# Kernel tuning notes

Hardware: AMD Instinct MI355X
Metric: run time of the kernel (lower is better)

The kernel has to match this reference:

```python
import jax, jax.numpy as jnp
import numpy as np

EPSILON = 0.1      # entropic regularization
N_ITERS = 50       # Sinkhorn fixed-point iterations
EPS_STAB = 1e-6    # numerical stabilizer (max(eps_stab, 1e-6) in original)
N, M, D = 8192, 8192, 128


def _sinkhorn_cost(X, Y):
    # squared Euclidean cost matrix (n, m)
    x2 = jnp.sum(X * X, axis=-1)
    y2 = jnp.sum(Y * Y, axis=-1)
    C = jnp.maximum(x2[:, None] + y2[None, :] - 2.0 * (X @ Y.T), 0.0)
    K = jnp.exp(-C / EPSILON)
    n, m = X.shape[0], Y.shape[0]
    a = jnp.full((n,), 1.0 / n, dtype=C.dtype)
    b = jnp.full((m,), 1.0 / m, dtype=C.dtype)

    def step(uv, _):
        u, v = uv
        Kv = K @ v + EPS_STAB
        u = jnp.where(jnp.abs(Kv) < EPS_STAB, a, a / jnp.maximum(Kv, EPS_STAB))
        Ktu = K.T @ u + EPS_STAB
        v = jnp.where(jnp.abs(Ktu) < EPS_STAB, b, b / jnp.maximum(Ktu, EPS_STAB))
        return (u, v), None

    (u, v), _ = jax.lax.scan(step, (jnp.ones_like(a), jnp.ones_like(b)), None, length=N_ITERS)
    # cost = sum(pi * C) with pi = u[:,None] * K * v[None,:], fused via einsum
    return jnp.einsum('i,ij,ij,j->', u, K, C, v)


def setup_inputs() -> dict:
    key = jax.random.key(0)
    k1, k2 = jax.random.split(key)
    # scale so squared distances ~O(1), commensurate with EPSILON
    X = jax.random.normal(k1, (N, D), dtype=jnp.float32) * 0.05
    Y = jax.random.normal(k2, (M, D), dtype=jnp.float32) * 0.05
    return {"X": X, "Y": Y}


def reference(X, Y):
    ot_xy = _sinkhorn_cost(X, Y)
    ot_xx = _sinkhorn_cost(X, jax.lax.stop_gradient(X))
    ot_yy = _sinkhorn_cost(Y, jax.lax.stop_gradient(Y))
    div = ot_xy - 0.5 * (ot_xx + ot_yy)
    div = jnp.where(jnp.isfinite(div), div, jnp.zeros_like(div))
    return jnp.maximum(div, 0.0)
```

## Files before the change

### kernel.cpp

```cpp
#include <hip/hip_runtime.h>

#define NPTS 8192
#define DIM  128
#define WPREP(x) (0.015625f / ((x) + 1.28e-4f))

typedef short s16x8 __attribute__((ext_vector_type(8)));
typedef float f32x4 __attribute__((ext_vector_type(4)));
typedef float f32x2 __attribute__((ext_vector_type(2)));

__device__ __forceinline__ ushort f2bf(float f) {
  unsigned u = __float_as_uint(f);
  u += 0x7fffu + ((u >> 16) & 1u);
  return (ushort)(u >> 16);
}
__device__ __forceinline__ float bf2f(ushort b) {
  return __uint_as_float(((unsigned)b) << 16);
}

__device__ __forceinline__ unsigned char fp8_enc_sw(float f) {
  if (f < 0.015625f) {
    int mi = (int)rintf(f * 512.0f);
    return (unsigned char)(mi >= 8 ? 0x08 : mi);
  }
  unsigned u = __float_as_uint(f);
  unsigned r = u + 0xfffffu + ((u >> 20) & 1u);
  int e = (int)((r >> 23) & 0xff) - 127;
  unsigned mant = (r >> 20) & 7u;
  if (e > 8 || (e == 8 && mant > 6)) return 0x7e;
  return (unsigned char)(((e + 7) << 3) | mant);
}
__device__ __forceinline__ float fp8_dec_sw(unsigned b) {
  unsigned E = (b >> 3) & 15u, M = b & 7u;
  float n = __uint_as_float(((E + 120u) << 23) | (M << 20));
  float s = (float)M * 0.001953125f;
  return E ? n : s;
}
__device__ __forceinline__ unsigned char enc1(float f) {
#if __has_builtin(__builtin_amdgcn_cvt_pk_fp8_f32)
  return (unsigned char)(__builtin_amdgcn_cvt_pk_fp8_f32(f, f, 0, false) & 0xff);
#else
  return fp8_enc_sw(f);
#endif
}
template <bool HI>
__device__ __forceinline__ f32x2 dec2(unsigned w) {
#if __has_builtin(__builtin_amdgcn_cvt_pk_f32_fp8)
  return __builtin_amdgcn_cvt_pk_f32_fp8((int)w, HI);
#else
  f32x2 r;
  r.x = fp8_dec_sw(HI ? ((w >> 16) & 0xffu) : (w & 0xffu));
  r.y = fp8_dec_sw(HI ? (w >> 24) : ((w >> 8) & 0xffu));
  return r;
#endif
}

__device__ __forceinline__ int swz(int j) { return j + 2 * (j >> 5); }
#define WSZ (NPTS + 2 * (NPTS / 32) + 8)

__global__ __launch_bounds__(256) void init_zero2(float* __restrict__ a,
                                                  float* __restrict__ b) {
  int j = blockIdx.x * 256 + threadIdx.x;
  a[j] = 0.0f; b[j] = 0.0f;
}

__global__ __launch_bounds__(256) void sq_rows(const float* __restrict__ X,
                                               const float* __restrict__ Y,
                                               float* __restrict__ x2,
                                               float* __restrict__ y2) {
  int wave = threadIdx.x >> 6, lane = threadIdx.x & 63;
  int row = blockIdx.x * 4 + wave;
  const float* src = (row < NPTS) ? X + (size_t)row * DIM
                                  : Y + (size_t)(row - NPTS) * DIM;
  float2 v = *reinterpret_cast<const float2*>(src + lane * 2);
  float ax = bf2f(f2bf(v.x)), ay = bf2f(f2bf(v.y));
  float s = ax * ax + ay * ay;
  for (int off = 32; off; off >>= 1) s += __shfl_down(s, off, 64);
  if (lane == 0) {
    if (row < NPTS) x2[row] = s; else y2[row - NPTS] = s;
  }
}

__global__ __launch_bounds__(256) void build_k(const float* __restrict__ A,
                                               const float* __restrict__ B,
                                               const float* __restrict__ a2,
                                               const float* __restrict__ b2,
                                               unsigned char* __restrict__ K8) {
  __shared__ ushort At[128][136];
  __shared__ ushort Bt[128][136];
  int t = threadIdx.x;
  int tm = blockIdx.x, tn = blockIdx.y;
  {
    int r = t >> 1;
    int c0 = (t & 1) * 64;
    const float* Ar = A + (size_t)(tm * 128 + r) * DIM + c0;
    const float* Br = B + (size_t)(tn * 128 + r) * DIM + c0;
    for (int c = 0; c < 64; c += 4) {
      float4 av = *reinterpret_cast<const float4*>(Ar + c);
      float4 bv = *reinterpret_cast<const float4*>(Br + c);
      unsigned pa0 = (unsigned)f2bf(av.x) | ((unsigned)f2bf(av.y) << 16);
      unsigned pa1 = (unsigned)f2bf(av.z) | ((unsigned)f2bf(av.w) << 16);
      unsigned pb0 = (unsigned)f2bf(bv.x) | ((unsigned)f2bf(bv.y) << 16);
      unsigned pb1 = (unsigned)f2bf(bv.z) | ((unsigned)f2bf(bv.w) << 16);
      *reinterpret_cast<unsigned*>(&At[r][c0 + c + 0]) = pa0;
      *reinterpret_cast<unsigned*>(&At[r][c0 + c + 2]) = pa1;
      *reinterpret_cast<unsigned*>(&Bt[r][c0 + c + 0]) = pb0;
      *reinterpret_cast<unsigned*>(&Bt[r][c0 + c + 2]) = pb1;
    }
  }
  __syncthreads();
  int wave = t >> 6, lane = t & 63;
  int lr = lane & 15;
  int lk = (lane >> 4) * 8;
  f32x4 acc[2][8];
  for (int mi = 0; mi < 2; ++mi)
    for (int ni = 0; ni < 8; ++ni)
      acc[mi][ni] = (f32x4){0.f, 0.f, 0.f, 0.f};
  for (int kc = 0; kc < 4; ++kc) {
    s16x8 af[2], bfr[8];
    af[0] = *reinterpret_cast<const s16x8*>(&At[wave * 32 + lr][kc * 32 + lk]);
    af[1] = *reinterpret_cast<const s16x8*>(&At[wave * 32 + 16 + lr][kc * 32 + lk]);
    for (int ni = 0; ni < 8; ++ni)
      bfr[ni] = *reinterpret_cast<const s16x8*>(&Bt[ni * 16 + lr][kc * 32 + lk]);
    for (int mi = 0; mi < 2; ++mi)
      for (int ni = 0; ni < 8; ++ni)
        acc[mi][ni] = __builtin_amdgcn_mfma_f32_16x16x32_bf16(af[mi], bfr[ni],
                                                              acc[mi][ni], 0, 0, 0);
  }
  int drow = (lane >> 4) * 4;
  float a2r[2][4], b2c[8];
  for (int mi = 0; mi < 2; ++mi)
    for (int r = 0; r < 4; ++r) a2r[mi][r] = a2[tm * 128 + wave * 32 + mi * 16 + drow + r];
  for (int ni = 0; ni < 8; ++ni) b2c[ni] = b2[tn * 128 + ni * 16 + lr];
  __syncthreads();
  unsigned char (*O)[144] = reinterpret_cast<unsigned char (*)[144]>(&At[0][0]);
  for (int mi = 0; mi < 2; ++mi)
    for (int ni = 0; ni < 8; ++ni)
      for (int r = 0; r < 4; ++r) {
        float S = acc[mi][ni][r];
        float C = fmaxf(a2r[mi][r] + b2c[ni] - 2.0f * S, 0.0f);
        float kv = exp2f(7.0f - 14.426950408889634f * C);
        O[wave * 32 + mi * 16 + drow + r][ni * 16 + lr] = enc1(kv);
      }
  __syncthreads();
  int row = t >> 1, half = t & 1;
  const uint4* src = reinterpret_cast<const uint4*>(&O[row][half * 64]);
  uint4* dst = reinterpret_cast<uint4*>(K8 + (size_t)(tm * 128 + row) * NPTS + tn * 128 + half * 64);
#pragma unroll
  for (int k = 0; k < 4; ++k) dst[k] = src[k];
}

struct SymMem {
  unsigned char T[128][132];
  float wj[128], wi[128];
  float cp[8][128];
};

__device__ __forceinline__ void sym_tile(const unsigned char* __restrict__ K8,
                                         const float* __restrict__ in,
                                         float* __restrict__ acc,
                                         float* __restrict__ zn,
                                         int tid, int init, SymMem& sm) {
  int t = threadIdx.x;
  if (tid < 32) zn[tid * 256 + t] = 0.0f;
  int bi = (int)(64.5f - sqrtf(64.5f * 64.5f - 2.0f * (float)tid));
  if (bi < 0) bi = 0; if (bi > 63) bi = 63;
  while (bi > 0 && tid < bi * 64 - bi * (bi - 1) / 2) --bi;
  while (tid >= (bi + 1) * 64 - (bi + 1) * bi / 2) ++bi;
  int bj = bi + tid - (bi * 64 - bi * (bi - 1) / 2);
  if (t < 128) sm.wj[t] = init ? 1.0f : WPREP(in[bj * 128 + t]);
  else         sm.wi[t - 128] = init ? 1.0f : WPREP(in[bi * 128 + (t - 128)]);
  int r = t >> 1, h = t & 1;
  const unsigned char* src = K8 + (size_t)(bi * 128 + r) * NPTS + bj * 128 + h * 64;
  uint4 q[4];
#pragma unroll
  for (int k = 0; k < 4; ++k) q[k] = *reinterpret_cast<const uint4*>(src + 16 * k);
  bool offdiag = (bi != bj);
  if (offdiag) {
#pragma unroll
    for (int k = 0; k < 4; ++k)
      *reinterpret_cast<uint4*>(&sm.T[r][h * 64 + 16 * k]) = q[k];
  }
  __syncthreads();
  float racc = 0.f;
#pragma unroll
  for (int k = 0; k < 4; ++k) {
    const unsigned* p = &q[k].x;
#pragma unroll
    for (int e = 0; e < 4; ++e) {
      f32x2 lo = dec2<false>(p[e]), hi2 = dec2<true>(p[e]);
      int c = h * 64 + k * 16 + e * 4;
      racc = fmaf(lo.x, sm.wj[c], racc);
      racc = fmaf(lo.y, sm.wj[c + 1], racc);
      racc = fmaf(hi2.x, sm.wj[c + 2], racc);
      racc = fmaf(hi2.y, sm.wj[c + 3], racc);
    }
  }
  racc += __shfl_xor(racc, 1, 64);
  if (h == 0) atomicAdd(&acc[bi * 128 + r], racc);
  if (offdiag) {
    int cg = t >> 3, rg = t & 7;
    float c0 = 0.f, c1 = 0.f, c2 = 0.f, c3 = 0.f;
#pragma unroll
    for (int i = 0; i < 16; ++i) {
      int row = rg * 16 + ((i + rg * 2) & 15);
      unsigned v = *reinterpret_cast<const unsigned*>(&sm.T[row][cg * 4]);
      float wr = sm.wi[row];
      f32x2 lo = dec2<false>(v), hi2 = dec2<true>(v);
      c0 = fmaf(lo.x, wr, c0);
      c1 = fmaf(lo.y, wr, c1);
      c2 = fmaf(hi2.x, wr, c2);
      c3 = fmaf(hi2.y, wr, c3);
    }
    *reinterpret_cast<float4*>(&sm.cp[rg][cg * 4]) = make_float4(c0, c1, c2, c3);
    __syncthreads();
    if (t < 128) {
      float s = (((sm.cp[0][t] + sm.cp[1][t]) + (sm.cp[2][t] + sm.cp[3][t])) +
                 ((sm.cp[4][t] + sm.cp[5][t]) + (sm.cp[6][t] + sm.cp[7][t])));
      atomicAdd(&acc[bj * 128 + t], s);
    }
  }
}

__device__ __forceinline__ void row_block(const unsigned char* __restrict__ K8,
                                          float* __restrict__ out,
                                          int row0, int t, const float* w) {
  int lane = t & 63;
  const unsigned char* K0 = K8 + (size_t)row0 * NPTS + lane * 16;
  const unsigned char* K1 = K0 + NPTS;
  float a0 = 0.f, b0 = 0.f, a1 = 0.f, b1 = 0.f;
  uint4 c0 = *reinterpret_cast<const uint4*>(K0);
  uint4 c1 = *reinterpret_cast<const uint4*>(K1);
#pragma unroll
  for (int rnd = 0; rnd < 8; ++rnd) {
    uint4 n0 = c0, n1 = c1;
    if (rnd < 7) {
      n0 = *reinterpret_cast<const uint4*>(K0 + (rnd + 1) * 1024);
      n1 = *reinterpret_cast<const uint4*>(K1 + (rnd + 1) * 1024);
    }
    int pb = swz(rnd * 1024 + lane * 16);
    const unsigned* p0 = &c0.x;
    const unsigned* p1 = &c1.x;
#pragma unroll
    for (int e = 0; e < 4; ++e) {
      f32x2 w0 = *reinterpret_cast<const f32x2*>(&w[pb + 4 * e]);
      f32x2 w1 = *reinterpret_cast<const f32x2*>(&w[pb + 4 * e + 2]);
      f32x2 k0l = dec2<false>(p0[e]), k0h = dec2<true>(p0[e]);
      f32x2 k1l = dec2<false>(p1[e]), k1h = dec2<true>(p1[e]);
      a0 = fmaf(k0l.x, w0.x, a0); b0 = fmaf(k0l.y, w0.y, b0);
      a0 = fmaf(k0h.x, w1.x, a0); b0 = fmaf(k0h.y, w1.y, b0);
      a1 = fmaf(k1l.x, w0.x, a1); b1 = fmaf(k1l.y, w0.y, b1);
      a1 = fmaf(k1h.x, w1.x, a1); b1 = fmaf(k1h.y, w1.y, b1);
    }
    c0 = n0; c1 = n1;
  }
  float s0 = a0 + b0, s1 = a1 + b1;
  for (int off = 32; off; off >>= 1) {
    s0 += __shfl_down(s0, off, 64);
    s1 += __shfl_down(s1, off, 64);
  }
  if (lane == 0) { out[row0] = s0; out[row0 + 1] = s1; }
}

union MegaMem {
  SymMem sym;
  float w[WSZ];
  float us[64];
};

__global__ __launch_bounds__(256) void megapass(const unsigned char* __restrict__ KA,
                                                const unsigned char* __restrict__ KB,
                                                const unsigned char* __restrict__ KXY,
                                                const float* __restrict__ inA,
                                                const float* __restrict__ inB,
                                                float* __restrict__ accA,
                                                float* __restrict__ accB,
                                                float* __restrict__ znA,
                                                float* __restrict__ znB,
                                                const float* __restrict__ xyin,
                                                float* __restrict__ rxy,
                                                float* __restrict__ vabn,
                                                int p, int xyrole) {
  __shared__ MegaMem sm;
  int bx = blockIdx.x;
  int t = threadIdx.x;
  bool isxy = (bx % 5 == 4) && (bx < 5120);
  if (isxy) {
    int xyi = bx / 5;
    if (xyrole == 0) {
      if (t < 8) vabn[xyi * 8 + t] = 0.0f;
      if (p == 1) {
#pragma unroll
        for (int k = 0; k < 32; ++k) sm.w[swz(t + 256 * k)] = 1.0f;
      } else {
        float tmp[32];
#pragma unroll
        for (int k = 0; k < 32; ++k) tmp[k] = xyin[t + 256 * k];
#pragma unroll
        for (int k = 0; k < 32; ++k) sm.w[swz(t + 256 * k)] = WPREP(tmp[k]);
      }
      __syncthreads();
      int row0 = xyi * 8 + (t >> 6) * 2;
      row_block(KXY, rxy, row0, t, sm.w);
    } else {
      int jb = xyi & 7, ic = xyi >> 3;
      int i0 = ic * 64;
      if (t < 64) sm.us[t] = WPREP(rxy[i0 + t]);
      __syncthreads();
      int j0 = jb * 1024 + t * 4;
      float acc0 = 0.f, acc1 = 0.f, acc2 = 0.f, acc3 = 0.f;
      for (int i = 0; i < 64; i += 8) {
        unsigned wv[8];
#pragma unroll
        for (int k = 0; k < 8; ++k)
          wv[k] = *reinterpret_cast<const unsigned*>(KXY + (size_t)(i0 + i + k) * NPTS + j0);
#pragma unroll
        for (int k = 0; k < 8; ++k) {
          float uu = sm.us[i + k];
          f32x2 lo = dec2<false>(wv[k]), hi = dec2<true>(wv[k]);
          acc0 = fmaf(lo.x, uu, acc0);
          acc1 = fmaf(lo.y, uu, acc1);
          acc2 = fmaf(hi.x, uu, acc2);
          acc3 = fmaf(hi.y, uu, acc3);
        }
      }
      atomicAdd(&vabn[j0 + 0], acc0);
      atomicAdd(&vabn[j0 + 1], acc1);
      atomicAdd(&vabn[j0 + 2], acc2);
      atomicAdd(&vabn[j0 + 3], acc3);
    }
  } else {
    int nxy_below = (bx < 5120) ? ((bx + 1) / 5) : 1024;
    int symi = bx - nxy_below;
    int half = symi & 1;
    int tid = symi >> 1;
    sym_tile(half ? KB : KA, half ? inB : inA, half ? accB : accA,
             half ? znB : znA, tid, p == 1 ? 1 : 0, sm.sym);
  }
}

__global__ __launch_bounds__(256) void sympass2(const unsigned char* __restrict__ KA,
                                                const unsigned char* __restrict__ KB,
                                                const float* __restrict__ inA,
                                                const float* __restrict__ inB,
                                                float* __restrict__ accA,
                                                float* __restrict__ accB,
                                                float* __restrict__ znA,
                                                float* __restrict__ znB,
                                                int init) {
  __shared__ SymMem sm;
  int half = blockIdx.y;
  sym_tile(half ? KB : KA, half ? inB : inA, half ? accB : accA,
           half ? znB : znA, blockIdx.x, init, sm);
}

__device__ __forceinline__ void prep_w512(float* w, const float* __restrict__ in, int init, int t) {
  if (init) {
#pragma unroll
    for (int k = 0; k < 16; ++k) w[swz(t + 512 * k)] = 1.0f;
  } else {
    float tmp[16];
#pragma unroll
    for (int k = 0; k < 16; ++k) tmp[k] = in[t + 512 * k];
#pragma unroll
    for (int k = 0; k < 16; ++k) w[swz(t + 512 * k)] = WPREP(tmp[k]);
  }
}

__global__ __launch_bounds__(512) void rowpass_xy(const unsigned char* __restrict__ K8,
                                                  const float* __restrict__ in,
                                                  float* __restrict__ out,
                                                  float* __restrict__ vzero,
                                                  int init) {
  __shared__ float w[WSZ];
  int t = threadIdx.x;
  if (t < 16) vzero[blockIdx.x * 16 + t] = 0.0f;
  prep_w512(w, in, init, t);
  __syncthreads();
  int row0 = blockIdx.x * 16 + (t >> 6) * 2;
  row_block(K8, out, row0, t, w);
}

__global__ __launch_bounds__(256) void colpass(const unsigned char* __restrict__ K8,
                                               const float* __restrict__ uraw,
                                               float* __restrict__ vout) {
  __shared__ float us[64];
  int t = threadIdx.x;
  int jb = blockIdx.x;
  int ic = blockIdx.y;
  int i0 = ic * 64;
  if (t < 64) us[t] = WPREP(uraw[i0 + t]);
  __syncthreads();
  int j0 = jb * 1024 + t * 4;
  float acc0 = 0.f, acc1 = 0.f, acc2 = 0.f, acc3 = 0.f;
  for (int i = 0; i < 64; i += 8) {
    unsigned wv[8];
#pragma unroll
    for (int k = 0; k < 8; ++k)
      wv[k] = *reinterpret_cast<const unsigned*>(K8 + (size_t)(i0 + i + k) * NPTS + j0);
#pragma unroll
    for (int k = 0; k < 8; ++k) {
      float uu = us[i + k];
      f32x2 lo = dec2<false>(wv[k]), hi = dec2<true>(wv[k]);
      acc0 = fmaf(lo.x, uu, acc0);
      acc1 = fmaf(lo.y, uu, acc1);
      acc2 = fmaf(hi.x, uu, acc2);
      acc3 = fmaf(hi.y, uu, acc3);
    }
  }
  atomicAdd(&vout[j0 + 0], acc0);
  atomicAdd(&vout[j0 + 1], acc1);
  atomicAdd(&vout[j0 + 2], acc2);
  atomicAdd(&vout[j0 + 3], acc3);
}

__global__ __launch_bounds__(256) void costpass(const unsigned char* __restrict__ K8,
                                                const float* __restrict__ uraw,
                                                const float* __restrict__ vraw,
                                                float* __restrict__ partial) {
  __shared__ float w[WSZ];
  __shared__ float wsum[4];
  int t = threadIdx.x;
  {
    float tmp[32];
#pragma unroll
    for (int k = 0; k < 32; ++k) tmp[k] = vraw[t + 256 * k];
#pragma unroll
    for (int k = 0; k < 32; ++k) w[swz(t + 256 * k)] = WPREP(tmp[k]);
  }
  __syncthreads();
  int wave = t >> 6, lane = t & 63;
  int row = blockIdx.x * 4 + wave;
  const unsigned char* Kr = K8 + (size_t)row * NPTS + lane * 16;
  float acc = 0.f;
  uint4 c = *reinterpret_cast<const uint4*>(Kr);
#pragma unroll
  for (int rnd = 0; rnd < 8; ++rnd) {
    uint4 n = c;
    if (rnd < 7) n = *reinterpret_cast<const uint4*>(Kr + (rnd + 1) * 1024);
    const unsigned* p = &c.x;
    int pb = swz(rnd * 1024 + lane * 16);
#pragma unroll
    for (int e = 0; e < 4; ++e) {
      f32x2 w0 = *reinterpret_cast<const f32x2*>(&w[pb + 4 * e]);
      f32x2 w1 = *reinterpret_cast<const f32x2*>(&w[pb + 4 * e + 2]);
      f32x2 kl = dec2<false>(p[e]), kh = dec2<true>(p[e]);
      float c0 = (kl.x > 0.f) ? 0.069314718f * (7.0f - __log2f(kl.x)) : 0.f;
      float c1 = (kl.y > 0.f) ? 0.069314718f * (7.0f - __log2f(kl.y)) : 0.f;
      float c2 = (kh.x > 0.f) ? 0.069314718f * (7.0f - __log2f(kh.x)) : 0.f;
      float c3 = (kh.y > 0.f) ? 0.069314718f * (7.0f - __log2f(kh.y)) : 0.f;
      acc = fmaf(kl.x * c0, w0.x, acc);
      acc = fmaf(kl.y * c1, w0.y, acc);
      acc = fmaf(kh.x * c2, w1.x, acc);
      acc = fmaf(kh.y * c3, w1.y, acc);
    }
    c = n;
  }
  for (int off = 32; off; off >>= 1) acc += __shfl_down(acc, off, 64);
  if (lane == 0) {
    float u = WPREP(uraw[row]);
    wsum[wave] = acc * u * 0.0078125f;
  }
  __syncthreads();
  if (t == 0) partial[blockIdx.x] = (wsum[0] + wsum[1]) + (wsum[2] + wsum[3]);
}

__global__ __launch_bounds__(256) void final_combine(const float* __restrict__ pxy,
                                                     const float* __restrict__ pxx,
                                                     const float* __restrict__ pyy,
                                                     float* __restrict__ out) {
  __shared__ float buf[3][256];
  int t = threadIdx.x;
  float s0 = 0.f, s1 = 0.f, s2 = 0.f;
  for (int i = t; i < 2048; i += 256) { s0 += pxy[i]; s1 += pxx[i]; s2 += pyy[i]; }
  buf[0][t] = s0; buf[1][t] = s1; buf[2][t] = s2;
  __syncthreads();
  for (int off = 128; off; off >>= 1) {
    if (t < off) {
      buf[0][t] += buf[0][t + off];
      buf[1][t] += buf[1][t + off];
      buf[2][t] += buf[2][t + off];
    }
    __syncthreads();
  }
  if (t == 0) {
    float div = buf[0][0] - 0.5f * (buf[1][0] + buf[2][0]);
    if (!isfinite(div)) div = 0.0f;
    out[0] = fmaxf(div, 0.0f);
  }
}

extern "C" void kernel_launch(void* const* d_in, const int* in_sizes, int n_in,
                              void* d_out, int out_size, void* d_ws, size_t ws_size,
                              hipStream_t stream) {
  const float* X = (const float*)d_in[0];
  const float* Y = (const float*)d_in[1];
  float* out = (float*)d_out;
  char* ws = (char*)d_ws;

  size_t off = 0;
  unsigned char* KA = (unsigned char*)(ws + off); off += (size_t)NPTS * NPTS;
  unsigned char* KB = (unsigned char*)(ws + off); off += (size_t)NPTS * NPTS;
  float* zA[3]; float* zB[3];
  for (int i = 0; i < 3; ++i) { zA[i] = (float*)(ws + off); off += (size_t)NPTS * 4; }
  for (int i = 0; i < 3; ++i) { zB[i] = (float*)(ws + off); off += (size_t)NPTS * 4; }
  float* rxy  = (float*)(ws + off); off += (size_t)NPTS * 4;
  float* vab0 = (float*)(ws + off); off += (size_t)NPTS * 4;
  float* vab1 = (float*)(ws + off); off += (size_t)NPTS * 4;
  float* x2   = (float*)(ws + off); off += (size_t)NPTS * 4;
  float* y2   = (float*)(ws + off); off += (size_t)NPTS * 4;
  float* pxy  = (float*)(ws + off); off += 2048 * 4;
  float* pxx  = (float*)(ws + off); off += 2048 * 4;
  float* pyy  = (float*)(ws + off); off += 2048 * 4;
  size_t need_base = off;
  unsigned char* KXY = (unsigned char*)(ws + off); off += (size_t)NPTS * NPTS;
  bool fused = (ws_size >= off);
  if (ws_size < need_base) {
    (void)hipMemsetAsync(d_out, 0, sizeof(float), stream);
    return;
  }
  float* vab[2] = {vab0, vab1};

  init_zero2<<<32, 256, 0, stream>>>(zA[1], zB[1]);
  sq_rows<<<4096, 256, 0, stream>>>(X, Y, x2, y2);

  if (fused) {
    build_k<<<dim3(64, 64), 256, 0, stream>>>(X, X, x2, x2, KA);
    build_k<<<dim3(64, 64), 256, 0, stream>>>(Y, Y, y2, y2, KB);
    build_k<<<dim3(64, 64), 256, 0, stream>>>(X, Y, x2, y2, KXY);
    for (int k = 0; k < 100; ++k) {
      int p = k + 1;
      int it = k >> 1;
      int role = k & 1;
      megapass<<<5184, 256, 0, stream>>>(KA, KB, KXY,
                                         zA[(p - 1) % 3], zB[(p - 1) % 3],
                                         zA[p % 3], zB[p % 3],
                                         zA[(p + 1) % 3], zB[(p + 1) % 3],
                                         vab[it & 1], rxy, vab[(it + 1) & 1],
                                         p, role);
    }
    costpass<<<2048, 256, 0, stream>>>(KA, zA[0], zA[1], pxx);
    costpass<<<2048, 256, 0, stream>>>(KB, zB[0], zB[1], pyy);
    costpass<<<2048, 256, 0, stream>>>(KXY, rxy, vab[0], pxy);
  } else {
    build_k<<<dim3(64, 64), 256, 0, stream>>>(X, X, x2, x2, KA);
    build_k<<<dim3(64, 64), 256, 0, stream>>>(Y, Y, y2, y2, KB);
    for (int p = 1; p <= 100; ++p) {
      sympass2<<<dim3(2080, 2), 256, 0, stream>>>(KA, KB,
                                                  zA[(p - 1) % 3], zB[(p - 1) % 3],
                                                  zA[p % 3], zB[p % 3],
                                                  zA[(p + 1) % 3], zB[(p + 1) % 3],
                                                  p == 1 ? 1 : 0);
    }
    costpass<<<2048, 256, 0, stream>>>(KA, zA[0], zA[1], pxx);
    costpass<<<2048, 256, 0, stream>>>(KB, zB[0], zB[1], pyy);
    build_k<<<dim3(64, 64), 256, 0, stream>>>(X, Y, x2, y2, KA);
    for (int it = 0; it < 50; ++it) {
      rowpass_xy<<<512, 512, 0, stream>>>(KA, vab[it & 1], rxy,
                                          vab[(it + 1) & 1], it == 0 ? 1 : 0);
      colpass<<<dim3(8, 128), 256, 0, stream>>>(KA, rxy, vab[(it + 1) & 1]);
    }
    costpass<<<2048, 256, 0, stream>>>(KA, rxy, vab[0], pxy);
  }

  final_combine<<<1, 256, 0, stream>>>(pxy, pxx, pyy, out);
}
```

Baseline: 3.312 ms.

## Chunk XY weight staging in LDS, add occupancy hint, and XOR-swizzle build_k tiles

The XY row-block path of megapass no longer stages the full 8192-entry weight vector in shared memory. It now streams it in double-buffered 2048-entry chunks, interleaving the weight loads with the FP8 K row dot products. This shrinks LDS use, and together with a launch_bounds minimum-blocks hint of 6 it aims to raise occupancy for the memory-bound sweeps, at the cost of extra barriers. Separately, build_k XOR-swizzles the bf16 tile columns in LDS to reduce bank conflicts on the MFMA fragment loads.

```diff
diff --git a/kernel.cpp b/kernel.cpp
--- a/kernel.cpp
+++ b/kernel.cpp
@@ -56,6 +56,7 @@
 
 __device__ __forceinline__ int swz(int j) { return j + 2 * (j >> 5); }
 #define WSZ (NPTS + 2 * (NPTS / 32) + 8)
+#define CHSZ 2176
 
 __global__ __launch_bounds__(256) void init_zero2(float* __restrict__ a,
                                                   float* __restrict__ b) {
@@ -92,6 +93,7 @@
   {
     int r = t >> 1;
     int c0 = (t & 1) * 64;
+    int xr = (r & 7) << 4;
     const float* Ar = A + (size_t)(tm * 128 + r) * DIM + c0;
     const float* Br = B + (size_t)(tn * 128 + r) * DIM + c0;
     for (int c = 0; c < 64; c += 4) {
@@ -101,26 +103,29 @@
       unsigned pa1 = (unsigned)f2bf(av.z) | ((unsigned)f2bf(av.w) << 16);
       unsigned pb0 = (unsigned)f2bf(bv.x) | ((unsigned)f2bf(bv.y) << 16);
       unsigned pb1 = (unsigned)f2bf(bv.z) | ((unsigned)f2bf(bv.w) << 16);
-      *reinterpret_cast<unsigned*>(&At[r][c0 + c + 0]) = pa0;
-      *reinterpret_cast<unsigned*>(&At[r][c0 + c + 2]) = pa1;
-      *reinterpret_cast<unsigned*>(&Bt[r][c0 + c + 0]) = pb0;
-      *reinterpret_cast<unsigned*>(&Bt[r][c0 + c + 2]) = pb1;
+      int cc = (c0 + c) ^ xr;
+      *reinterpret_cast<unsigned*>(&At[r][cc + 0]) = pa0;
+      *reinterpret_cast<unsigned*>(&At[r][cc + 2]) = pa1;
+      *reinterpret_cast<unsigned*>(&Bt[r][cc + 0]) = pb0;
+      *reinterpret_cast<unsigned*>(&Bt[r][cc + 2]) = pb1;
     }
   }
   __syncthreads();
   int wave = t >> 6, lane = t & 63;
   int lr = lane & 15;
   int lk = (lane >> 4) * 8;
+  int xs = (lr & 7) << 4;
   f32x4 acc[2][8];
   for (int mi = 0; mi < 2; ++mi)
     for (int ni = 0; ni < 8; ++ni)
       acc[mi][ni] = (f32x4){0.f, 0.f, 0.f, 0.f};
   for (int kc = 0; kc < 4; ++kc) {
+    int ck = (kc * 32 + lk) ^ xs;
     s16x8 af[2], bfr[8];
-    af[0] = *reinterpret_cast<const s16x8*>(&At[wave * 32 + lr][kc * 32 + lk]);
-    af[1] = *reinterpret_cast<const s16x8*>(&At[wave * 32 + 16 + lr][kc * 32 + lk]);
+    af[0] = *reinterpret_cast<const s16x8*>(&At[wave * 32 + lr][ck]);
+    af[1] = *reinterpret_cast<const s16x8*>(&At[wave * 32 + 16 + lr][ck]);
     for (int ni = 0; ni < 8; ++ni)
-      bfr[ni] = *reinterpret_cast<const s16x8*>(&Bt[ni * 16 + lr][kc * 32 + lk]);
+      bfr[ni] = *reinterpret_cast<const s16x8*>(&Bt[ni * 16 + lr][ck]);
     for (int mi = 0; mi < 2; ++mi)
       for (int ni = 0; ni < 8; ++ni)
         acc[mi][ni] = __builtin_amdgcn_mfma_f32_16x16x32_bf16(af[mi], bfr[ni],
@@ -263,23 +268,23 @@
 
 union MegaMem {
   SymMem sym;
-  float w[WSZ];
+  float wch[2][CHSZ];
   float us[64];
 };
 
-__global__ __launch_bounds__(256) void megapass(const unsigned char* __restrict__ KA,
-                                                const unsigned char* __restrict__ KB,
-                                                const unsigned char* __restrict__ KXY,
-                                                const float* __restrict__ inA,
-                                                const float* __restrict__ inB,
-                                                float* __restrict__ accA,
-                                                float* __restrict__ accB,
-                                                float* __restrict__ znA,
-                                                float* __restrict__ znB,
-                                                const float* __restrict__ xyin,
-                                                float* __restrict__ rxy,
-                                                float* __restrict__ vabn,
-                                                int p, int xyrole) {
+__global__ __launch_bounds__(256, 6) void megapass(const unsigned char* __restrict__ KA,
+                                                   const unsigned char* __restrict__ KB,
+                                                   const unsigned char* __restrict__ KXY,
+                                                   const float* __restrict__ inA,
+                                                   const float* __restrict__ inB,
+                                                   float* __restrict__ accA,
+                                                   float* __restrict__ accB,
+                                                   float* __restrict__ znA,
+                                                   float* __restrict__ znB,
+                                                   const float* __restrict__ xyin,
+                                                   float* __restrict__ rxy,
+                                                   float* __restrict__ vabn,
+                                                   int p, int xyrole) {
   __shared__ MegaMem sm;
   int bx = blockIdx.x;
   int t = threadIdx.x;
@@ -288,19 +293,73 @@
     int xyi = bx / 5;
     if (xyrole == 0) {
       if (t < 8) vabn[xyi * 8 + t] = 0.0f;
+      int lane = t & 63;
+      int row0 = xyi * 8 + (t >> 6) * 2;
+      const unsigned char* K0 = KXY + (size_t)row0 * NPTS + lane * 16;
+      const unsigned char* K1 = K0 + NPTS;
       if (p == 1) {
 #pragma unroll
-        for (int k = 0; k < 32; ++k) sm.w[swz(t + 256 * k)] = 1.0f;
+        for (int k = 0; k < 8; ++k) sm.wch[0][swz(t + 256 * k)] = 1.0f;
       } else {
-        float tmp[32];
-#pragma unroll
-        for (int k = 0; k < 32; ++k) tmp[k] = xyin[t + 256 * k];
-#pragma unroll
-        for (int k = 0; k < 32; ++k) sm.w[swz(t + 256 * k)] = WPREP(tmp[k]);
+        float tmp[8];
+#pragma unroll
+        for (int k = 0; k < 8; ++k) tmp[k] = xyin[t + 256 * k];
+#pragma unroll
+        for (int k = 0; k < 8; ++k) sm.wch[0][swz(t + 256 * k)] = WPREP(tmp[k]);
       }
       __syncthreads();
-      int row0 = xyi * 8 + (t >> 6) * 2;
-      row_block(KXY, rxy, row0, t, sm.w);
+      float a0 = 0.f, b0 = 0.f, a1 = 0.f, b1 = 0.f;
+      uint4 c0v = *reinterpret_cast<const uint4*>(K0);
+      uint4 c1v = *reinterpret_cast<const uint4*>(K1);
+#pragma unroll
+      for (int ch = 0; ch < 4; ++ch) {
+        if (ch < 3) {
+          float* wb = sm.wch[(ch + 1) & 1];
+          int base = (ch + 1) * 2048;
+          if (p == 1) {
+#pragma unroll
+            for (int k = 0; k < 8; ++k) wb[swz(t + 256 * k)] = 1.0f;
+          } else {
+            float tmp[8];
+#pragma unroll
+            for (int k = 0; k < 8; ++k) tmp[k] = xyin[base + t + 256 * k];
+#pragma unroll
+            for (int k = 0; k < 8; ++k) wb[swz(t + 256 * k)] = WPREP(tmp[k]);
+          }
+        }
+        const float* w = sm.wch[ch & 1];
+#pragma unroll
+        for (int rr = 0; rr < 2; ++rr) {
+          int rnd = ch * 2 + rr;
+          uint4 n0 = c0v, n1 = c1v;
+          if (rnd < 7) {
+            n0 = *reinterpret_cast<const uint4*>(K0 + (rnd + 1) * 1024);
+            n1 = *reinterpret_cast<const uint4*>(K1 + (rnd + 1) * 1024);
+          }
+          int pb = swz(rr * 1024 + lane * 16);
+          const unsigned* p0 = &c0v.x;
+          const unsigned* p1 = &c1v.x;
+#pragma unroll
+          for (int e = 0; e < 4; ++e) {
+            f32x2 w0 = *reinterpret_cast<const f32x2*>(&w[pb + 4 * e]);
+            f32x2 w1 = *reinterpret_cast<const f32x2*>(&w[pb + 4 * e + 2]);
+            f32x2 k0l = dec2<false>(p0[e]), k0h = dec2<true>(p0[e]);
+            f32x2 k1l = dec2<false>(p1[e]), k1h = dec2<true>(p1[e]);
+            a0 = fmaf(k0l.x, w0.x, a0); b0 = fmaf(k0l.y, w0.y, b0);
+            a0 = fmaf(k0h.x, w1.x, a0); b0 = fmaf(k0h.y, w1.y, b0);
+            a1 = fmaf(k1l.x, w0.x, a1); b1 = fmaf(k1l.y, w0.y, b1);
+            a1 = fmaf(k1h.x, w1.x, a1); b1 = fmaf(k1h.y, w1.y, b1);
+          }
+          c0v = n0; c1v = n1;
+        }
+        __syncthreads();
+      }
+      float s0 = a0 + b0, s1 = a1 + b1;
+      for (int off = 32; off; off >>= 1) {
+        s0 += __shfl_down(s0, off, 64);
+        s1 += __shfl_down(s1, off, 64);
+      }
+      if (lane == 0) { rxy[row0] = s0; rxy[row0 + 1] = s1; }
     } else {
       int jb = xyi & 7, ic = xyi >> 3;
       int i0 = ic * 64;
```

New measurement: 3.400 ms. +2.7%, slower.

## Exploit symmetry: build and cost only upper-triangular tiles of self kernels

Applied to the files above, without the earlier changes.

The self-similarity kernels KA and KB are now built over only the 2080 upper-triangular 128x128 tiles instead of all 4096, since the sym passes read only those tiles. A new symmetric cost pass reads each triangular tile once and accumulates both the row and transposed column contributions, with the off-diagonal tiles counted twice. An XOR swizzle is also added to the LDS layout in the shared build tile to reduce bank conflicts on MFMA operand loads. The lower triangle of KA and KB is left unwritten, which is safe only if nothing else reads it.

```diff
diff --git a/kernel.cpp b/kernel.cpp
--- a/kernel.cpp
+++ b/kernel.cpp
@@ -56,6 +56,15 @@
 
 __device__ __forceinline__ int swz(int j) { return j + 2 * (j >> 5); }
 #define WSZ (NPTS + 2 * (NPTS / 32) + 8)
+
+__device__ __forceinline__ void tri_decode(int tid, int& bi, int& bj) {
+  int b = (int)(64.5f - sqrtf(64.5f * 64.5f - 2.0f * (float)tid));
+  if (b < 0) b = 0; if (b > 63) b = 63;
+  while (b > 0 && tid < b * 64 - b * (b - 1) / 2) --b;
+  while (tid >= (b + 1) * 64 - (b + 1) * b / 2) ++b;
+  bi = b;
+  bj = b + tid - (b * 64 - b * (b - 1) / 2);
+}
 
 __global__ __launch_bounds__(256) void init_zero2(float* __restrict__ a,
                                                   float* __restrict__ b) {
@@ -80,18 +89,18 @@
   }
 }
 
-__global__ __launch_bounds__(256) void build_k(const float* __restrict__ A,
-                                               const float* __restrict__ B,
-                                               const float* __restrict__ a2,
-                                               const float* __restrict__ b2,
-                                               unsigned char* __restrict__ K8) {
-  __shared__ ushort At[128][136];
-  __shared__ ushort Bt[128][136];
-  int t = threadIdx.x;
-  int tm = blockIdx.x, tn = blockIdx.y;
+__device__ __forceinline__ void build_tile(const float* __restrict__ A,
+                                           const float* __restrict__ B,
+                                           const float* __restrict__ a2,
+                                           const float* __restrict__ b2,
+                                           unsigned char* __restrict__ K8,
+                                           int tm, int tn,
+                                           ushort (*At)[136], ushort (*Bt)[136]) {
+  int t = threadIdx.x;
   {
     int r = t >> 1;
     int c0 = (t & 1) * 64;
+    int xr = (r & 7) << 4;
     const float* Ar = A + (size_t)(tm * 128 + r) * DIM + c0;
     const float* Br = B + (size_t)(tn * 128 + r) * DIM + c0;
     for (int c = 0; c < 64; c += 4) {
@@ -101,26 +110,29 @@
       unsigned pa1 = (unsigned)f2bf(av.z) | ((unsigned)f2bf(av.w) << 16);
       unsigned pb0 = (unsigned)f2bf(bv.x) | ((unsigned)f2bf(bv.y) << 16);
       unsigned pb1 = (unsigned)f2bf(bv.z) | ((unsigned)f2bf(bv.w) << 16);
-      *reinterpret_cast<unsigned*>(&At[r][c0 + c + 0]) = pa0;
-      *reinterpret_cast<unsigned*>(&At[r][c0 + c + 2]) = pa1;
-      *reinterpret_cast<unsigned*>(&Bt[r][c0 + c + 0]) = pb0;
-      *reinterpret_cast<unsigned*>(&Bt[r][c0 + c + 2]) = pb1;
+      int cc = (c0 + c) ^ xr;
+      *reinterpret_cast<unsigned*>(&At[r][cc + 0]) = pa0;
+      *reinterpret_cast<unsigned*>(&At[r][cc + 2]) = pa1;
+      *reinterpret_cast<unsigned*>(&Bt[r][cc + 0]) = pb0;
+      *reinterpret_cast<unsigned*>(&Bt[r][cc + 2]) = pb1;
     }
   }
   __syncthreads();
   int wave = t >> 6, lane = t & 63;
   int lr = lane & 15;
   int lk = (lane >> 4) * 8;
+  int xs = (lr & 7) << 4;
   f32x4 acc[2][8];
   for (int mi = 0; mi < 2; ++mi)
     for (int ni = 0; ni < 8; ++ni)
       acc[mi][ni] = (f32x4){0.f, 0.f, 0.f, 0.f};
   for (int kc = 0; kc < 4; ++kc) {
+    int ck = (kc * 32 + lk) ^ xs;
     s16x8 af[2], bfr[8];
-    af[0] = *reinterpret_cast<const s16x8*>(&At[wave * 32 + lr][kc * 32 + lk]);
-    af[1] = *reinterpret_cast<const s16x8*>(&At[wave * 32 + 16 + lr][kc * 32 + lk]);
+    af[0] = *reinterpret_cast<const s16x8*>(&At[wave * 32 + lr][ck]);
+    af[1] = *reinterpret_cast<const s16x8*>(&At[wave * 32 + 16 + lr][ck]);
     for (int ni = 0; ni < 8; ++ni)
-      bfr[ni] = *reinterpret_cast<const s16x8*>(&Bt[ni * 16 + lr][kc * 32 + lk]);
+      bfr[ni] = *reinterpret_cast<const s16x8*>(&Bt[ni * 16 + lr][ck]);
     for (int mi = 0; mi < 2; ++mi)
       for (int ni = 0; ni < 8; ++ni)
         acc[mi][ni] = __builtin_amdgcn_mfma_f32_16x16x32_bf16(af[mi], bfr[ni],
@@ -149,6 +161,26 @@
   for (int k = 0; k < 4; ++k) dst[k] = src[k];
 }
 
+__global__ __launch_bounds__(256) void build_k(const float* __restrict__ A,
+                                               const float* __restrict__ B,
+                                               const float* __restrict__ a2,
+                                               const float* __restrict__ b2,
+                                               unsigned char* __restrict__ K8) {
+  __shared__ ushort At[128][136];
+  __shared__ ushort Bt[128][136];
+  build_tile(A, B, a2, b2, K8, blockIdx.x, blockIdx.y, At, Bt);
+}
+
+__global__ __launch_bounds__(256) void build_tri(const float* __restrict__ A,
+                                                 const float* __restrict__ a2,
+                                                 unsigned char* __restrict__ K8) {
+  __shared__ ushort At[128][136];
+  __shared__ ushort Bt[128][136];
+  int bi, bj;
+  tri_decode(blockIdx.x, bi, bj);
+  build_tile(A, A, a2, a2, K8, bi, bj, At, Bt);
+}
+
 struct SymMem {
   unsigned char T[128][132];
   float wj[128], wi[128];
@@ -162,11 +194,8 @@
                                          int tid, int init, SymMem& sm) {
   int t = threadIdx.x;
   if (tid < 32) zn[tid * 256 + t] = 0.0f;
-  int bi = (int)(64.5f - sqrtf(64.5f * 64.5f - 2.0f * (float)tid));
-  if (bi < 0) bi = 0; if (bi > 63) bi = 63;
-  while (bi > 0 && tid < bi * 64 - bi * (bi - 1) / 2) --bi;
-  while (tid >= (bi + 1) * 64 - (bi + 1) * bi / 2) ++bi;
-  int bj = bi + tid - (bi * 64 - bi * (bi - 1) / 2);
+  int bi, bj;
+  tri_decode(tid, bi, bj);
   if (t < 128) sm.wj[t] = init ? 1.0f : WPREP(in[bj * 128 + t]);
   else         sm.wi[t - 128] = init ? 1.0f : WPREP(in[bi * 128 + (t - 128)]);
   int r = t >> 1, h = t & 1;
@@ -464,6 +493,98 @@
   if (t == 0) partial[blockIdx.x] = (wsum[0] + wsum[1]) + (wsum[2] + wsum[3]);
 }
 
+__global__ __launch_bounds__(256) void costpass_sym(const unsigned char* __restrict__ K8,
+                                                    const float* __restrict__ uraw,
+                                                    const float* __restrict__ vraw,
+                                                    float* __restrict__ partial) {
+  __shared__ unsigned char T[128][132];
+  __shared__ float wui[128], wuj[128], wvi[128], wvj[128];
+  __shared__ float cp[8][128];
+  __shared__ float rsum[4], csum[4];
+  int tid = blockIdx.x;
+  int t = threadIdx.x;
+  int bi, bj;
+  tri_decode(tid, bi, bj);
+  if (t < 128) {
+    wvj[t] = WPREP(vraw[bj * 128 + t]);
+    wuj[t] = WPREP(uraw[bj * 128 + t]);
+  } else {
+    int i = t - 128;
+    wui[i] = WPREP(uraw[bi * 128 + i]);
+    wvi[i] = WPREP(vraw[bi * 128 + i]);
+  }
+  int r = t >> 1, h = t & 1;
+  const unsigned char* src = K8 + (size_t)(bi * 128 + r) * NPTS + bj * 128 + h * 64;
+  uint4 q[4];
+#pragma unroll
+  for (int k = 0; k < 4; ++k) q[k] = *reinterpret_cast<const uint4*>(src + 16 * k);
+  bool offdiag = (bi != bj);
+  if (offdiag) {
+#pragma unroll
+    for (int k = 0; k < 4; ++k)
+      *reinterpret_cast<uint4*>(&T[r][h * 64 + 16 * k]) = q[k];
+  }
+  __syncthreads();
+  int lane = t & 63, wave = t >> 6;
+  float racc = 0.f;
+#pragma unroll
+  for (int k = 0; k < 4; ++k) {
+    const unsigned* p = &q[k].x;
+#pragma unroll
+    for (int e = 0; e < 4; ++e) {
+      f32x2 lo = dec2<false>(p[e]), hi2 = dec2<true>(p[e]);
+      int c = h * 64 + k * 16 + e * 4;
+      float c0 = (lo.x > 0.f) ? 0.069314718f * (7.0f - __log2f(lo.x)) : 0.f;
+      float c1 = (lo.y > 0.f) ? 0.069314718f * (7.0f - __log2f(lo.y)) : 0.f;
+      float c2 = (hi2.x > 0.f) ? 0.069314718f * (7.0f - __log2f(hi2.x)) : 0.f;
+      float c3 = (hi2.y > 0.f) ? 0.069314718f * (7.0f - __log2f(hi2.y)) : 0.f;
+      racc = fmaf(lo.x * c0, wvj[c], racc);
+      racc = fmaf(lo.y * c1, wvj[c + 1], racc);
+      racc = fmaf(hi2.x * c2, wvj[c + 2], racc);
+      racc = fmaf(hi2.y * c3, wvj[c + 3], racc);
+    }
+  }
+  racc += __shfl_xor(racc, 1, 64);
+  float val = (h == 0) ? wui[r] * racc : 0.0f;
+  for (int off = 32; off; off >>= 1) val += __shfl_down(val, off, 64);
+  if (lane == 0) rsum[wave] = val;
+  if (offdiag) {
+    int cg = t >> 3, rg = t & 7;
+    float c0 = 0.f, c1 = 0.f, c2 = 0.f, c3 = 0.f;
+#pragma unroll
+    for (int i = 0; i < 16; ++i) {
+      int row = rg * 16 + ((i + rg * 2) & 15);
+      unsigned v = *reinterpret_cast<const unsigned*>(&T[row][cg * 4]);
+      float wr = wvi[row];
+      f32x2 lo = dec2<false>(v), hi2 = dec2<true>(v);
+      float d0 = (lo.x > 0.f) ? 0.069314718f * (7.0f - __log2f(lo.x)) : 0.f;
+      float d1 = (lo.y > 0.f) ? 0.069314718f * (7.0f - __log2f(lo.y)) : 0.f;
+      float d2 = (hi2.x > 0.f) ? 0.069314718f * (7.0f - __log2f(hi2.x)) : 0.f;
+      float d3 = (hi2.y > 0.f) ? 0.069314718f * (7.0f - __log2f(hi2.y)) : 0.f;
+      c0 = fmaf(lo.x * d0, wr, c0);
+      c1 = fmaf(lo.y * d1, wr, c1);
+      c2 = fmaf(hi2.x * d2, wr, c2);
+      c3 = fmaf(hi2.y * d3, wr, c3);
+    }
+    *reinterpret_cast<float4*>(&cp[rg][cg * 4]) = make_float4(c0, c1, c2, c3);
+    __syncthreads();
+    float colval = 0.f;
+    if (t < 128) {
+      float s = (((cp[0][t] + cp[1][t]) + (cp[2][t] + cp[3][t])) +
+                 ((cp[4][t] + cp[5][t]) + (cp[6][t] + cp[7][t])));
+      colval = wuj[t] * s;
+    }
+    for (int off = 32; off; off >>= 1) colval += __shfl_down(colval, off, 64);
+    if (lane == 0) csum[wave] = colval;
+  } else {
+    if (t < 4) csum[t] = 0.0f;
+  }
+  __syncthreads();
+  if (t == 0)
+    partial[tid] = 0.0078125f * (((rsum[0] + rsum[1]) + (rsum[2] + rsum[3])) +
+                                 ((csum[0] + csum[1]) + (csum[2] + csum[3])));
+}
+
 __global__ __launch_bounds__(256) void final_combine(const float* __restrict__ pxy,
                                                      const float* __restrict__ pxx,
                                                      const float* __restrict__ pyy,
@@ -471,7 +592,10 @@
   __shared__ float buf[3][256];
   int t = threadIdx.x;
   float s0 = 0.f, s1 = 0.f, s2 = 0.f;
-  for (int i = t; i < 2048; i += 256) { s0 += pxy[i]; s1 += pxx[i]; s2 += pyy[i]; }
+  for (int i = t; i < 2080; i += 256) {
+    if (i < 2048) s0 += pxy[i];
+    s1 += pxx[i]; s2 += pyy[i];
+  }
   buf[0][t] = s0; buf[1][t] = s1; buf[2][t] = s2;
   __syncthreads();
   for (int off = 128; off; off >>= 1) {
@@ -509,8 +633,8 @@
   float* x2   = (float*)(ws + off); off += (size_t)NPTS * 4;
   float* y2   = (float*)(ws + off); off += (size_t)NPTS * 4;
   float* pxy  = (float*)(ws + off); off += 2048 * 4;
-  float* pxx  = (float*)(ws + off); off += 2048 * 4;
-  float* pyy  = (float*)(ws + off); off += 2048 * 4;
+  float* pxx  = (float*)(ws + off); off += 2080 * 4;
+  float* pyy  = (float*)(ws + off); off += 2080 * 4;
   size_t need_base = off;
   unsigned char* KXY = (unsigned char*)(ws + off); off += (size_t)NPTS * NPTS;
   bool fused = (ws_size >= off);
@@ -524,8 +648,8 @@
   sq_rows<<<4096, 256, 0, stream>>>(X, Y, x2, y2);
 
   if (fused) {
-    build_k<<<dim3(64, 64), 256, 0, stream>>>(X, X, x2, x2, KA);
-    build_k<<<dim3(64, 64), 256, 0, stream>>>(Y, Y, y2, y2, KB);
+    build_tri<<<2080, 256, 0, stream>>>(X, x2, KA);
+    build_tri<<<2080, 256, 0, stream>>>(Y, y2, KB);
     build_k<<<dim3(64, 64), 256, 0, stream>>>(X, Y, x2, y2, KXY);
     for (int k = 0; k < 100; ++k) {
       int p = k + 1;
@@ -538,12 +662,12 @@
                                          vab[it & 1], rxy, vab[(it + 1) & 1],
                                          p, role);
     }
-    costpass<<<2048, 256, 0, stream>>>(KA, zA[0], zA[1], pxx);
-    costpass<<<2048, 256, 0, stream>>>(KB, zB[0], zB[1], pyy);
+    costpass_sym<<<2080, 256, 0, stream>>>(KA, zA[0], zA[1], pxx);
+    costpass_sym<<<2080, 256, 0, stream>>>(KB, zB[0], zB[1], pyy);
     costpass<<<2048, 256, 0, stream>>>(KXY, rxy, vab[0], pxy);
   } else {
-    build_k<<<dim3(64, 64), 256, 0, stream>>>(X, X, x2, x2, KA);
-    build_k<<<dim3(64, 64), 256, 0, stream>>>(Y, Y, y2, y2, KB);
+    build_tri<<<2080, 256, 0, stream>>>(X, x2, KA);
+    build_tri<<<2080, 256, 0, stream>>>(Y, y2, KB);
     for (int p = 1; p <= 100; ++p) {
       sympass2<<<dim3(2080, 2), 256, 0, stream>>>(KA, KB,
                                                   zA[(p - 1) % 3], zB[(p - 1) % 3],
@@ -551,8 +675,8 @@
                                                   zA[(p + 1) % 3], zB[(p + 1) % 3],
                                                   p == 1 ? 1 : 0);
     }
-    costpass<<<2048, 256, 0, stream>>>(KA, zA[0], zA[1], pxx);
-    costpass<<<2048, 256, 0, stream>>>(KB, zB[0], zB[1], pyy);
+    costpass_sym<<<2080, 256, 0, stream>>>(KA, zA[0], zA[1], pxx);
+    costpass_sym<<<2080, 256, 0, stream>>>(KB, zB[0], zB[1], pyy);
     build_k<<<dim3(64, 64), 256, 0, stream>>>(X, Y, x2, y2, KA);
     for (int it = 0; it < 50; ++it) {
       rowpass_xy<<<512, 512, 0, stream>>>(KA, vab[it & 1], rxy,
```

Measured after the change: 3.226 ms. 2.6% less time.
